# Kernel tuning notes

Measured on AMD Instinct MI355X. Metric: run time of the kernel, lower is better.

Reference implementation:

```python
import math
import jax, jax.numpy as jnp
import numpy as np

H = 16          # num_attention_heads
DH = 64         # attention_head_size
D = H * DH      # hidden_size
MAX_POS = 1024  # max_position_embeddings


def setup_inputs() -> dict:
    key = jax.random.key(0)
    ks = jax.random.split(key, 9)
    B, S = 8, 1024
    scale = 0.02
    return {
        "hidden_states": jax.random.normal(ks[0], (B, S, D), dtype=jnp.float32),
        "attention_mask": jnp.zeros((B, 1, 1, S), dtype=jnp.float32),
        "Wq": jax.random.normal(ks[1], (D, D), dtype=jnp.float32) * scale,
        "bq": jnp.zeros((D,), dtype=jnp.float32),
        "Wk": jax.random.normal(ks[2], (D, D), dtype=jnp.float32) * scale,
        "bk": jnp.zeros((D,), dtype=jnp.float32),
        "Wv": jax.random.normal(ks[3], (D, D), dtype=jnp.float32) * scale,
        "bv": jnp.zeros((D,), dtype=jnp.float32),
        "dist_emb": jax.random.normal(ks[4], (2 * MAX_POS - 1, DH), dtype=jnp.float32) * scale,
    }


def reference(hidden_states, attention_mask, Wq, bq, Wk, bk, Wv, bv, dist_emb):
    B, S, _ = hidden_states.shape
    # projections -> [B, H, S, DH]
    def heads(x):
        return x.reshape(B, S, H, DH).transpose(0, 2, 1, 3)
    q = heads(hidden_states @ Wq + bq)
    k = heads(hidden_states @ Wk + bk)
    v = heads(hidden_states @ Wv + bv)

    # fp32_cast_query_key == 'manual': cast q,k to fp32 before matmul (already fp32 here)
    scores = jnp.einsum("bhld,bhrd->bhlr", q.astype(jnp.float32), k.astype(jnp.float32))
    scores = scores / math.sqrt(DH)

    # relative_key_query positional bias
    pos = jnp.arange(S)
    distance = pos[:, None] - pos[None, :] + (MAX_POS - 1)   # [S, S]
    pe = dist_emb[distance].astype(q.dtype)                   # [S, S, DH]
    scores = scores + jnp.einsum("bhld,lrd->bhlr", q, pe) \
                     + jnp.einsum("bhrd,lrd->bhlr", k, pe)

    scores = scores + attention_mask
    # fp32_cast_attention_scores=True: softmax in fp32
    probs = jax.nn.softmax(scores.astype(jnp.float32), axis=-1).astype(hidden_states.dtype)

    ctx = jnp.einsum("bhlr,bhrd->bhld", probs, v)  # [B, H, S, DH]
    ctx = ctx.transpose(0, 2, 1, 3).reshape(B, S, D)
    return ctx
```

## Files before the change

### kernel.cpp

```cpp
#include <hip/hip_runtime.h>
#include <stdint.h>

typedef unsigned short u16;
typedef short bf16x8 __attribute__((ext_vector_type(8)));
typedef float f32x4 __attribute__((ext_vector_type(4)));
typedef u16 u16x8 __attribute__((ext_vector_type(8)));
typedef u16 u16x4 __attribute__((ext_vector_type(4)));

#define NB 8
#define NS 1024
#define NH 16
#define NDH 64
#define ND 1024

#define AS1 __attribute__((address_space(1)))
#define AS3 __attribute__((address_space(3)))

__device__ __forceinline__ int SWZ(int row, int colbyte){
  return (row << 7) + (colbyte ^ ((row & 7) << 4));
}

__device__ __forceinline__ u16 f2b(float x){
  unsigned u = __float_as_uint(x);
  u += 0x7FFFu + ((u >> 16) & 1u);
  return (u16)(u >> 16);
}
__device__ __forceinline__ float b2f(u16 h){ return __uint_as_float(((unsigned)h) << 16); }

__global__ void cast_f32_bf16(const float* __restrict__ in, u16* __restrict__ out, long n){
  long i = ((long)blockIdx.x * blockDim.x + threadIdx.x) * 8;
  if (i + 8 <= n){
    float4 a = *(const float4*)&in[i];
    float4 b = *(const float4*)&in[i + 4];
    u16x8 o;
    o[0]=f2b(a.x); o[1]=f2b(a.y); o[2]=f2b(a.z); o[3]=f2b(a.w);
    o[4]=f2b(b.x); o[5]=f2b(b.y); o[6]=f2b(b.z); o[7]=f2b(b.w);
    *(u16x8*)&out[i] = o;
  }
}

__global__ void transpose_w(const float* __restrict__ Wq, const float* __restrict__ Wk,
                            const float* __restrict__ Wv, u16* __restrict__ wt){
  __shared__ float tile[64][65];
  int p = blockIdx.z;
  const float* W = (p == 0) ? Wq : ((p == 1) ? Wk : Wv);
  int n0 = blockIdx.x * 64, k0 = blockIdx.y * 64;
  int t = threadIdx.x;
  int row = t >> 2, cb = (t & 3) * 16;
  #pragma unroll
  for (int cc = 0; cc < 4; ++cc){
    float4 v = *(const float4*)&W[(size_t)(k0 + row) * ND + n0 + cb + cc * 4];
    tile[row][cb + cc*4 + 0] = v.x; tile[row][cb + cc*4 + 1] = v.y;
    tile[row][cb + cc*4 + 2] = v.z; tile[row][cb + cc*4 + 3] = v.w;
  }
  __syncthreads();
  u16x8 o0, o1;
  #pragma unroll
  for (int kk = 0; kk < 8; ++kk) o0[kk] = f2b(tile[cb + kk][row]);
  #pragma unroll
  for (int kk = 0; kk < 8; ++kk) o1[kk] = f2b(tile[cb + 8 + kk][row]);
  size_t ob = ((size_t)(p * ND + n0 + row)) * ND + k0 + cb;
  *(u16x8*)&wt[ob]     = o0;
  *(u16x8*)&wt[ob + 8] = o1;
}

__global__ __launch_bounds__(256) void qkv_gemm(
    const u16* __restrict__ hsb, const u16* __restrict__ wtb,
    const float* __restrict__ bq, const float* __restrict__ bk, const float* __restrict__ bv,
    u16* __restrict__ qb, u16* __restrict__ kb, u16* __restrict__ vt){
  __shared__ __attribute__((aligned(16))) u16 Al[128 * 32];
  __shared__ __attribute__((aligned(16))) u16 Bl[128 * 32];
  int t = threadIdx.x;
  int lane = t & 63, w = t >> 6;
  int li = lane & 15, g = lane >> 4;
  int m0 = blockIdx.y * 128, n0 = blockIdx.x * 128;
  int wm = (w >> 1) * 64, wn = (w & 1) * 64;
  f32x4 acc[4][4];
  #pragma unroll
  for (int a = 0; a < 4; ++a)
    #pragma unroll
    for (int b = 0; b < 4; ++b){ f32x4 z = {0.f,0.f,0.f,0.f}; acc[a][b] = z; }

  for (int kt = 0; kt < 32; ++kt){
    __syncthreads();
    #pragma unroll
    for (int ph = 0; ph < 2; ++ph){
      int c = ph * 256 + t;
      int row = c >> 2, ch = c & 3;
      const u16* ga = &hsb[(size_t)(m0 + row) * ND + kt * 32 + ch * 8];
      __builtin_amdgcn_global_load_lds((const AS1 void*)ga,
          (AS3 void*)&Al[(ph * 256 + w * 64) * 8], 16, 0, 0);
      const u16* gb = &wtb[(size_t)(n0 + row) * ND + kt * 32 + ch * 8];
      __builtin_amdgcn_global_load_lds((const AS1 void*)gb,
          (AS3 void*)&Bl[(ph * 256 + w * 64) * 8], 16, 0, 0);
    }
    asm volatile("s_waitcnt vmcnt(0)" ::: "memory");
    __syncthreads();
    bf16x8 af[4], bfr[4];
    #pragma unroll
    for (int mt = 0; mt < 4; ++mt)
      af[mt] = *(const bf16x8*)&Al[(wm + mt * 16 + li) * 32 + g * 8];
    #pragma unroll
    for (int nt = 0; nt < 4; ++nt)
      bfr[nt] = *(const bf16x8*)&Bl[(wn + nt * 16 + li) * 32 + g * 8];
    #pragma unroll
    for (int mt = 0; mt < 4; ++mt)
      #pragma unroll
      for (int nt = 0; nt < 4; ++nt)
        acc[mt][nt] = __builtin_amdgcn_mfma_f32_16x16x32_bf16(af[mt], bfr[nt], acc[mt][nt], 0, 0, 0);
  }

  int proj = n0 >> 10;
  const float* bias = (proj == 0) ? bq : ((proj == 1) ? bk : bv);
  #pragma unroll
  for (int nt = 0; nt < 4; ++nt){
    int n = n0 + wn + nt * 16 + li;
    int nc = n & 1023;
    float bv_ = bias[nc];
    #pragma unroll
    for (int mt = 0; mt < 4; ++mt){
      #pragma unroll
      for (int r = 0; r < 4; ++r){
        int m = m0 + wm + mt * 16 + g * 4 + r;
        u16 hv = f2b(acc[mt][nt][r] + bv_);
        if (proj == 0)      qb[(size_t)m * ND + nc] = hv;
        else if (proj == 1) kb[(size_t)m * ND + nc] = hv;
        else {
          int bb = m >> 10, s = m & 1023;
          int hh = nc >> 6, dh = nc & 63;
          vt[((size_t)(bb * NH + hh) * NDH + dh) * NS + s] = hv;
        }
      }
    }
  }
}

__global__ __launch_bounds__(256, 3) void attn(
    const u16* __restrict__ qb, const u16* __restrict__ kb,
    const u16* __restrict__ vt, const u16* __restrict__ eb,
    const float* __restrict__ mask, float* __restrict__ out){
  __shared__ __attribute__((aligned(16))) u16 k_lds[64 * 72];
  __shared__ __attribute__((aligned(16))) u16 v_lds[64 * 72];
  __shared__ __attribute__((aligned(16))) u16 u2[128 * 64];
  __shared__ __attribute__((aligned(16))) u16 w2[128 * 64];

  int t = threadIdx.x, lane = t & 63, w = t >> 6;
  int li = lane & 15, g = lane >> 4;
  int lt = blockIdx.x, bh = blockIdx.y;
  int b = bh >> 4, h = bh & 15;
  int l0 = lt * 64;
  int iA  = w * 16 + g * 4;
  int iA2 = iA * 2;
  int li2 = li * 2;
  int ttc = iA + 63 - li;
  int colw = iA2;

  bf16x8 qf[2];
  {
    size_t qoff = ((size_t)(b * NS + l0 + w * 16 + li)) * ND + h * NDH;
    qf[0] = *(const bf16x8*)&qb[qoff + 0 + g * 8];
    qf[1] = *(const bf16x8*)&qb[qoff + 32 + g * 8];
  }
  f32x4 oacc[4];
  #pragma unroll
  for (int i = 0; i < 4; ++i){ f32x4 z = {0.f,0.f,0.f,0.f}; oacc[i] = z; }
  float mold[4] = {-1e30f, -1e30f, -1e30f, -1e30f};
  float lsum[4] = {0.f, 0.f, 0.f, 0.f};

  for (int kt2 = 0; kt2 < 16; ++kt2){
    int r0 = kt2 * 64;
    int ebase = l0 - r0 + 960;

    __syncthreads();
    {
      u16x8 rk[2], rv[2];
      #pragma unroll
      for (int ph = 0; ph < 2; ++ph){
        int c = ph * 256 + t, row = c >> 3, ch = c & 7;
        rk[ph] = *(const u16x8*)&kb[((size_t)(b * NS + r0 + row)) * ND + h * NDH + ch * 8];
        rv[ph] = *(const u16x8*)&vt[((size_t)(bh * NDH + row)) * NS + r0 + ch * 8];
      }
      #pragma unroll
      for (int ph = 0; ph < 2; ++ph){
        int c = ph * 256 + t, row = c >> 3, ch = c & 7;
        *(u16x8*)&k_lds[row * 72 + ch * 8] = rk[ph];
        *(u16x8*)&v_lds[row * 72 + ch * 8] = rv[ph];
      }
    }
    __syncthreads();

    bf16x8 kf[2];
    kf[0] = *(const bf16x8*)&k_lds[(w * 16 + li) * 72 + 0 + g * 8];
    kf[1] = *(const bf16x8*)&k_lds[(w * 16 + li) * 72 + 32 + g * 8];

    #pragma unroll
    for (int nt = 0; nt < 8; ++nt){
      int trow = nt * 16 + li;
      int er = ebase + trow; if (er > 2046) er = 2046;
      f32x4 ua = {0.f,0.f,0.f,0.f}, wa = {0.f,0.f,0.f,0.f};
      #pragma unroll
      for (int k2 = 0; k2 < 2; ++k2){
        bf16x8 ef = *(const bf16x8*)&eb[(size_t)er * NDH + k2 * 32 + g * 8];
        ua = __builtin_amdgcn_mfma_f32_16x16x32_bf16(qf[k2], ef, ua, 0, 0, 0);
        wa = __builtin_amdgcn_mfma_f32_16x16x32_bf16(kf[k2], ef, wa, 0, 0, 0);
      }
      u16x4 up, wp;
      #pragma unroll
      for (int r = 0; r < 4; ++r){ up[r] = f2b(ua[r]); wp[r] = f2b(wa[r]); }
      *(u16x4*)((char*)u2 + SWZ(trow, colw)) = up;
      *(u16x4*)((char*)w2 + SWZ(trow, colw)) = wp;
    }

    f32x4 sacc[4];
    #pragma unroll
    for (int jt = 0; jt < 4; ++jt){
      f32x4 z = {0.f,0.f,0.f,0.f}; sacc[jt] = z;
      #pragma unroll
      for (int k2 = 0; k2 < 2; ++k2){
        bf16x8 kbf = *(const bf16x8*)&k_lds[(jt * 16 + li) * 72 + k2 * 32 + g * 8];
        sacc[jt] = __builtin_amdgcn_mfma_f32_16x16x32_bf16(qf[k2], kbf, sacc[jt], 0, 0, 0);
      }
    }
    __syncthreads();

    float sv[4][4];
    #pragma unroll
    for (int jt = 0; jt < 4; ++jt){
      float mk = mask[b * NS + r0 + jt * 16 + li];
      int j2 = jt * 32 + li2;
      #pragma unroll
      for (int r = 0; r < 4; ++r){
        int tt = ttc + r - jt * 16;
        int byU = (tt << 7) + ((iA2 + 2 * r) ^ ((tt & 7) << 4));
        int byW = (tt << 7) + (j2 ^ ((tt & 7) << 4));
        float u  = b2f(*(const u16*)((const char*)u2 + byU));
        float ww = b2f(*(const u16*)((const char*)w2 + byW));
        sv[jt][r] = sacc[jt][r] * 0.125f + u + ww + mk;
      }
    }

    float rmax[4], rsum[4];
    #pragma unroll
    for (int r = 0; r < 4; ++r)
      rmax[r] = fmaxf(fmaxf(sv[0][r], sv[1][r]), fmaxf(sv[2][r], sv[3][r]));
    #pragma unroll
    for (int xm = 1; xm <= 8; xm <<= 1)
      #pragma unroll
      for (int r = 0; r < 4; ++r)
        rmax[r] = fmaxf(rmax[r], __shfl_xor(rmax[r], xm));
    float mnew[4], fac[4];
    #pragma unroll
    for (int r = 0; r < 4; ++r){
      mnew[r] = fmaxf(mold[r], rmax[r]);
      fac[r]  = __expf(mold[r] - mnew[r]);
    }
    float pr[4][4];
    #pragma unroll
    for (int r = 0; r < 4; ++r) rsum[r] = 0.f;
    #pragma unroll
    for (int jt = 0; jt < 4; ++jt)
      #pragma unroll
      for (int r = 0; r < 4; ++r){
        pr[jt][r] = __expf(sv[jt][r] - mnew[r]);
        rsum[r] += pr[jt][r];
      }
    #pragma unroll
    for (int xm = 1; xm <= 8; xm <<= 1)
      #pragma unroll
      for (int r = 0; r < 4; ++r)
        rsum[r] += __shfl_xor(rsum[r], xm);
    #pragma unroll
    for (int r = 0; r < 4; ++r){
      lsum[r] = lsum[r] * fac[r] + rsum[r];
      mold[r] = mnew[r];
    }
    #pragma unroll
    for (int nt2 = 0; nt2 < 4; ++nt2)
      #pragma unroll
      for (int r = 0; r < 4; ++r)
        oacc[nt2][r] *= fac[r];

    __syncthreads();
    #pragma unroll
    for (int jt = 0; jt < 4; ++jt)
      #pragma unroll
      for (int r = 0; r < 4; ++r){
        int prow = w * 16 + g * 4 + r;
        *(u16*)((char*)u2 + SWZ(prow, jt * 32 + li2)) = f2b(pr[jt][r]);
      }

    #pragma unroll
    for (int k2 = 0; k2 < 2; ++k2){
      bf16x8 pf = *(const bf16x8*)((const char*)u2 + SWZ(w * 16 + li, k2 * 64 + g * 16));
      #pragma unroll
      for (int nt2 = 0; nt2 < 4; ++nt2){
        bf16x8 vf = *(const bf16x8*)&v_lds[(nt2 * 16 + li) * 72 + k2 * 32 + g * 8];
        oacc[nt2] = __builtin_amdgcn_mfma_f32_16x16x32_bf16(pf, vf, oacc[nt2], 0, 0, 0);
      }
    }
  }

  #pragma unroll
  for (int nt2 = 0; nt2 < 4; ++nt2)
    #pragma unroll
    for (int r = 0; r < 4; ++r){
      int row = l0 + w * 16 + g * 4 + r;
      out[((size_t)(b * NS + row)) * ND + h * NDH + nt2 * 16 + li] = oacc[nt2][r] / lsum[r];
    }
}

extern "C" void kernel_launch(void* const* d_in, const int* in_sizes, int n_in,
                              void* d_out, int out_size, void* d_ws, size_t ws_size,
                              hipStream_t stream){
  (void)in_sizes; (void)n_in; (void)out_size; (void)ws_size;
  const float* hs   = (const float*)d_in[0];
  const float* mask = (const float*)d_in[1];
  const float* Wq   = (const float*)d_in[2];
  const float* bq   = (const float*)d_in[3];
  const float* Wk   = (const float*)d_in[4];
  const float* bk   = (const float*)d_in[5];
  const float* Wv   = (const float*)d_in[6];
  const float* bv   = (const float*)d_in[7];
  const float* de   = (const float*)d_in[8];
  float* out = (float*)d_out;
  char* ws = (char*)d_ws;

  u16* hsb = (u16*)(ws);
  u16* wtb = (u16*)(ws + 16777216);
  u16* eb  = (u16*)(ws + 23068672);
  u16* qb  = (u16*)(ws + 23330816);
  u16* kb  = (u16*)(ws + 40108032);
  u16* vt  = (u16*)(ws + 56885248);

  cast_f32_bf16<<<4096, 256, 0, stream>>>(hs, hsb, 8388608L);
  cast_f32_bf16<<<64, 256, 0, stream>>>(de, eb, 131008L);
  transpose_w<<<dim3(16, 16, 3), 256, 0, stream>>>(Wq, Wk, Wv, wtb);
  qkv_gemm<<<dim3(24, 64), 256, 0, stream>>>(hsb, wtb, bq, bk, bv, qb, kb, vt);
  attn<<<dim3(16, 128), 256, 0, stream>>>(qb, kb, vt, eb, mask, out);
}
```

Before: 493.9 us.

## Prefetch next K/V tile into registers and reuse overlapping distance-embedding rows

K and V tile loads for the next iteration are issued into registers right after the current tile is stored to LDS, so global latency overlaps with compute. The distance-embedding fragments are split into two halves. The high half of the current tile equals the low half of the previous tile, so it is carried over in registers and only four of the eight row blocks are fetched each iteration. The QK MFMAs are moved before the embedding MFMAs to hide the load latency. This costs more live registers, which may reduce occupancy.

```diff
diff --git a/kernel.cpp b/kernel.cpp
--- a/kernel.cpp
+++ b/kernel.cpp
@@ -161,6 +161,27 @@
     qf[0] = *(const bf16x8*)&qb[qoff + 0 + g * 8];
     qf[1] = *(const bf16x8*)&qb[qoff + 32 + g * 8];
   }
+
+  bf16x8 ehi[4][2];
+  #pragma unroll
+  for (int nt = 0; nt < 4; ++nt){
+    int er = l0 + 1024 + nt * 16 + li;
+    if (er > 2046) er = 2046;
+    #pragma unroll
+    for (int k2 = 0; k2 < 2; ++k2)
+      ehi[nt][k2] = *(const bf16x8*)&eb[(size_t)er * NDH + k2 * 32 + g * 8];
+  }
+
+  u16x8 rk[2], rv[2];
+  {
+    #pragma unroll
+    for (int ph = 0; ph < 2; ++ph){
+      int c = ph * 256 + t, row = c >> 3, ch = c & 7;
+      rk[ph] = *(const u16x8*)&kb[((size_t)(b * NS + row)) * ND + h * NDH + ch * 8];
+      rv[ph] = *(const u16x8*)&vt[((size_t)(bh * NDH + row)) * NS + ch * 8];
+    }
+  }
+
   f32x4 oacc[4];
   #pragma unroll
   for (int i = 0; i < 4; ++i){ f32x4 z = {0.f,0.f,0.f,0.f}; oacc[i] = z; }
@@ -172,37 +193,56 @@
     int ebase = l0 - r0 + 960;
 
     __syncthreads();
+    #pragma unroll
+    for (int ph = 0; ph < 2; ++ph){
+      int c = ph * 256 + t, row = c >> 3, ch = c & 7;
+      *(u16x8*)&k_lds[row * 72 + ch * 8] = rk[ph];
+      *(u16x8*)&v_lds[row * 72 + ch * 8] = rv[ph];
+    }
+    __syncthreads();
+
     {
-      u16x8 rk[2], rv[2];
+      int rn = ((kt2 + 1) & 15) * 64;
       #pragma unroll
       for (int ph = 0; ph < 2; ++ph){
         int c = ph * 256 + t, row = c >> 3, ch = c & 7;
-        rk[ph] = *(const u16x8*)&kb[((size_t)(b * NS + r0 + row)) * ND + h * NDH + ch * 8];
-        rv[ph] = *(const u16x8*)&vt[((size_t)(bh * NDH + row)) * NS + r0 + ch * 8];
-      }
-      #pragma unroll
-      for (int ph = 0; ph < 2; ++ph){
-        int c = ph * 256 + t, row = c >> 3, ch = c & 7;
-        *(u16x8*)&k_lds[row * 72 + ch * 8] = rk[ph];
-        *(u16x8*)&v_lds[row * 72 + ch * 8] = rv[ph];
-      }
-    }
-    __syncthreads();
+        rk[ph] = *(const u16x8*)&kb[((size_t)(b * NS + rn + row)) * ND + h * NDH + ch * 8];
+        rv[ph] = *(const u16x8*)&vt[((size_t)(bh * NDH + row)) * NS + rn + ch * 8];
+      }
+    }
+
+    bf16x8 elo[4][2];
+    #pragma unroll
+    for (int nt = 0; nt < 4; ++nt){
+      int er = ebase + nt * 16 + li;
+      #pragma unroll
+      for (int k2 = 0; k2 < 2; ++k2)
+        elo[nt][k2] = *(const bf16x8*)&eb[(size_t)er * NDH + k2 * 32 + g * 8];
+    }
 
     bf16x8 kf[2];
     kf[0] = *(const bf16x8*)&k_lds[(w * 16 + li) * 72 + 0 + g * 8];
     kf[1] = *(const bf16x8*)&k_lds[(w * 16 + li) * 72 + 32 + g * 8];
 
-    #pragma unroll
-    for (int nt = 0; nt < 8; ++nt){
+    f32x4 sacc[4];
+    #pragma unroll
+    for (int jt = 0; jt < 4; ++jt){
+      f32x4 z = {0.f,0.f,0.f,0.f}; sacc[jt] = z;
+      #pragma unroll
+      for (int k2 = 0; k2 < 2; ++k2){
+        bf16x8 kbf = *(const bf16x8*)&k_lds[(jt * 16 + li) * 72 + k2 * 32 + g * 8];
+        sacc[jt] = __builtin_amdgcn_mfma_f32_16x16x32_bf16(qf[k2], kbf, sacc[jt], 0, 0, 0);
+      }
+    }
+
+    #pragma unroll
+    for (int nt = 4; nt < 8; ++nt){
       int trow = nt * 16 + li;
-      int er = ebase + trow; if (er > 2046) er = 2046;
       f32x4 ua = {0.f,0.f,0.f,0.f}, wa = {0.f,0.f,0.f,0.f};
       #pragma unroll
       for (int k2 = 0; k2 < 2; ++k2){
-        bf16x8 ef = *(const bf16x8*)&eb[(size_t)er * NDH + k2 * 32 + g * 8];
-        ua = __builtin_amdgcn_mfma_f32_16x16x32_bf16(qf[k2], ef, ua, 0, 0, 0);
-        wa = __builtin_amdgcn_mfma_f32_16x16x32_bf16(kf[k2], ef, wa, 0, 0, 0);
+        ua = __builtin_amdgcn_mfma_f32_16x16x32_bf16(qf[k2], ehi[nt - 4][k2], ua, 0, 0, 0);
+        wa = __builtin_amdgcn_mfma_f32_16x16x32_bf16(kf[k2], ehi[nt - 4][k2], wa, 0, 0, 0);
       }
       u16x4 up, wp;
       #pragma unroll
@@ -210,16 +250,25 @@
       *(u16x4*)((char*)u2 + SWZ(trow, colw)) = up;
       *(u16x4*)((char*)w2 + SWZ(trow, colw)) = wp;
     }
-
-    f32x4 sacc[4];
-    #pragma unroll
-    for (int jt = 0; jt < 4; ++jt){
-      f32x4 z = {0.f,0.f,0.f,0.f}; sacc[jt] = z;
+    #pragma unroll
+    for (int nt = 0; nt < 4; ++nt){
+      int trow = nt * 16 + li;
+      f32x4 ua = {0.f,0.f,0.f,0.f}, wa = {0.f,0.f,0.f,0.f};
       #pragma unroll
       for (int k2 = 0; k2 < 2; ++k2){
-        bf16x8 kbf = *(const bf16x8*)&k_lds[(jt * 16 + li) * 72 + k2 * 32 + g * 8];
-        sacc[jt] = __builtin_amdgcn_mfma_f32_16x16x32_bf16(qf[k2], kbf, sacc[jt], 0, 0, 0);
-      }
+        ua = __builtin_amdgcn_mfma_f32_16x16x32_bf16(qf[k2], elo[nt][k2], ua, 0, 0, 0);
+        wa = __builtin_amdgcn_mfma_f32_16x16x32_bf16(kf[k2], elo[nt][k2], wa, 0, 0, 0);
+      }
+      u16x4 up, wp;
+      #pragma unroll
+      for (int r = 0; r < 4; ++r){ up[r] = f2b(ua[r]); wp[r] = f2b(wa[r]); }
+      *(u16x4*)((char*)u2 + SWZ(trow, colw)) = up;
+      *(u16x4*)((char*)w2 + SWZ(trow, colw)) = wp;
+    }
+    #pragma unroll
+    for (int nt = 0; nt < 4; ++nt){
+      ehi[nt][0] = elo[nt][0];
+      ehi[nt][1] = elo[nt][1];
     }
     __syncthreads();
 
```

Result: faster. 458.7 us (-7.1%).
